# Kernel optimization log

Measured on AMD Instinct MI355X. Metric: run time of the kernel, lower is better.

Reference implementation:

```python
import jax, jax.numpy as jnp
import numpy as np

B, S, D, H, DN, DR, R = 2, 2048, 2048, 16, 32, 32, 128
HD = DN + DR  # head_dim = 64
EPS = 1e-5


def rms_norm(x, w):
    ms = jnp.mean(x * x, axis=-1, keepdims=True)
    return w * (x * jax.lax.rsqrt(ms + EPS))


def rotate_half(x):
    x1, x2 = x[..., : x.shape[-1] // 2], x[..., x.shape[-1] // 2:]
    return jnp.concatenate([-x2, x1], axis=-1)


def apply_rope(q, k, cos, sin):
    cos = cos[None, None]  # [1,1,S,DR]
    sin = sin[None, None]
    return q * cos + rotate_half(q) * sin, k * cos + rotate_half(k) * sin


def setup_inputs() -> dict:
    key = jax.random.key(0)
    ks = jax.random.split(key, 11)
    x = jax.random.normal(ks[0], (B, S, D), dtype=jnp.float32)
    # rotary tables
    pos = jnp.arange(S, dtype=jnp.float32)
    inv_freq = 1.0 / (10000.0 ** (jnp.arange(0, DR, 2, dtype=jnp.float32) / DR))
    ang = pos[:, None] * inv_freq[None, :]          # [S, DR/2]
    emb = jnp.concatenate([ang, ang], axis=-1)      # [S, DR]
    cos, sin = jnp.cos(emb), jnp.sin(emb)
    # causal additive mask
    mask = jnp.where(jnp.tril(jnp.ones((S, S), bool)), 0.0, -1e9).astype(jnp.float32)[None, None]
    s = 0.02
    return {
        "x": x, "cos": cos, "sin": sin, "mask": mask,
        "w_kv_down": jax.random.normal(ks[1], (D, R)) * s,
        "kv_norm_w": jnp.ones((R,), jnp.float32),
        "w_uk": jax.random.normal(ks[2], (R, H * DN)) * s,
        "w_ur": jax.random.normal(ks[3], (R, H * DR)) * s,
        "w_uv": jax.random.normal(ks[4], (R, H * HD)) * s,
        "w_q_down": jax.random.normal(ks[5], (D, R)) * s,
        "q_norm_w": jnp.ones((R,), jnp.float32),
        "w_uq": jax.random.normal(ks[6], (R, H * DN)) * s,
        "w_qr": jax.random.normal(ks[7], (R, H * DR)) * s,
        "w_o": jax.random.normal(ks[8], (H * HD, D)) * s,
    }


def reference(x, cos, sin, mask, w_kv_down, kv_norm_w, w_uk, w_ur, w_uv,
              w_q_down, q_norm_w, w_uq, w_qr, w_o):
    b, s, _ = x.shape

    def heads(t, hd):  # [b,s,H*hd] -> [b,H,s,hd]
        return t.reshape(b, s, H, hd).transpose(0, 2, 1, 3)

    c_kv = rms_norm(x @ w_kv_down, kv_norm_w)      # [b,s,R]
    k_nope = heads(c_kv @ w_uk, DN)
    k_rope = heads(c_kv @ w_ur, DR)
    v = heads(c_kv @ w_uv, HD)

    c_q = rms_norm(x @ w_q_down, q_norm_w)
    q_nope = heads(c_q @ w_uq, DN)
    q_rope = heads(c_q @ w_qr, DR)

    q_rope, k_rope = apply_rope(q_rope, k_rope, cos, sin)
    q = jnp.concatenate([q_nope, q_rope], axis=-1)  # [b,H,s,HD]
    k = jnp.concatenate([k_nope, k_rope], axis=-1)

    scores = jnp.einsum('bhqd,bhkd->bhqk', q, k) / jnp.sqrt(jnp.float32(HD))
    scores = scores + mask
    attn = jax.nn.softmax(scores, axis=-1)
    out = jnp.einsum('bhqk,bhkd->bhqd', attn, v)    # [b,H,s,HD]
    out = out.transpose(0, 2, 1, 3).reshape(b, s, H * HD)
    return out @ w_o
```

## Files before the change

### kernel.cpp

```cpp
#include <hip/hip_runtime.h>
#include <hip/hip_bf16.h>


using short8   = __attribute__((ext_vector_type(8))) short;
using bf16x8   = __attribute__((ext_vector_type(8))) __bf16;
using f32x4    = __attribute__((ext_vector_type(4))) float;
using f32x16   = __attribute__((ext_vector_type(16))) float;
using u32x4    = __attribute__((ext_vector_type(4))) unsigned;
using ushort4v = __attribute__((ext_vector_type(4))) unsigned short;

#define DEV __device__ __forceinline__

DEV ushort f2bf(float f) {
  union { float f; unsigned u; } v; v.f = f;
  unsigned r = (v.u + 0x7FFFu + ((v.u >> 16) & 1u)) >> 16;
  return (ushort)r;
}
DEV float bf2f(ushort u) {
  union { unsigned u; float f; } v; v.u = ((unsigned)u) << 16;
  return v.f;
}
DEV f32x4 mfma16(short8 a, short8 b, f32x4 c) {
  return __builtin_amdgcn_mfma_f32_16x16x32_bf16(
      __builtin_bit_cast(bf16x8, a), __builtin_bit_cast(bf16x8, b), c, 0, 0, 0);
}
DEV f32x16 mfma32(short8 a, short8 b, f32x16 c) {
  return __builtin_amdgcn_mfma_f32_32x32x16_bf16(
      __builtin_bit_cast(bf16x8, a), __builtin_bit_cast(bf16x8, b), c, 0, 0, 0);
}
DEV unsigned packbf(float a, float b) {
  return (unsigned)f2bf(a) | ((unsigned)f2bf(b) << 16);
}
DEV short8 mk8(unsigned a, unsigned b, unsigned c, unsigned d) {
  u32x4 t; t[0] = a; t[1] = b; t[2] = c; t[3] = d;
  return __builtin_bit_cast(short8, t);
}
DEV float vmax16(f32x16 v) {
  float a0 = fmaxf(v[0], v[1]),  a1 = fmaxf(v[2], v[3]);
  float a2 = fmaxf(v[4], v[5]),  a3 = fmaxf(v[6], v[7]);
  float a4 = fmaxf(v[8], v[9]),  a5 = fmaxf(v[10], v[11]);
  float a6 = fmaxf(v[12], v[13]), a7 = fmaxf(v[14], v[15]);
  float b0 = fmaxf(a0, a1), b1 = fmaxf(a2, a3), b2 = fmaxf(a4, a5), b3 = fmaxf(a6, a7);
  return fmaxf(fmaxf(b0, b1), fmaxf(b2, b3));
}
DEV float vsum16(f32x16 v) {
  float a0 = v[0] + v[1],  a1 = v[2] + v[3];
  float a2 = v[4] + v[5],  a3 = v[6] + v[7];
  float a4 = v[8] + v[9],  a5 = v[10] + v[11];
  float a6 = v[12] + v[13], a7 = v[14] + v[15];
  float b0 = a0 + a1, b1 = a2 + a3, b2 = a4 + a5, b3 = a6 + a7;
  return (b0 + b1) + (b2 + b3);
}

#define GLD16(gp, lp)                                                        \
  __builtin_amdgcn_global_load_lds(                                          \
      (const __attribute__((address_space(1))) void*)(gp),                   \
      (__attribute__((address_space(3))) void*)(lp), 16, 0, 0)

__global__ __launch_bounds__(256) void k_cast_bf16(const float* __restrict__ src,
                                                   ushort* __restrict__ dst, int n4) {
  int i = blockIdx.x * 256 + threadIdx.x;
  if (i < n4) {
    float4 v = reinterpret_cast<const float4*>(src)[i];
    ushort4v o;
    o[0] = f2bf(v.x); o[1] = f2bf(v.y); o[2] = f2bf(v.z); o[3] = f2bf(v.w);
    reinterpret_cast<ushort4v*>(dst)[i] = o;
  }
}

__global__ __launch_bounds__(256) void k_ttile(ushort* __restrict__ dst, int ldD,
                                               const float* __restrict__ src, int ldS) {
  __shared__ float t[64][65];
  const int k0 = blockIdx.x * 64, n0 = blockIdx.y * 64;
  const int c = threadIdx.x & 63, r0 = threadIdx.x >> 6;
#pragma unroll
  for (int i = 0; i < 16; ++i) {
    int r = r0 + i * 4;
    t[r][c] = src[(size_t)(k0 + r) * ldS + n0 + c];
  }
  __syncthreads();
#pragma unroll
  for (int i = 0; i < 16; ++i) {
    int n = r0 + i * 4;
    dst[(size_t)(n0 + n) * ldD + k0 + c] = f2bf(t[c][n]);
  }
}

template <int OUT_BF16>
__global__ __launch_bounds__(256) void k_gemm128(const ushort* __restrict__ A,
                                                 const ushort* __restrict__ Bt,
                                                 void* __restrict__ Cv, int N, int K) {
  __shared__ ushort As[128 * 64];
  __shared__ ushort Bs[128 * 64];
  const int tid = threadIdx.x;
  const int lane = tid & 63, w = tid >> 6;
  const int wr = w >> 1, wc = w & 1;
  const int r15 = lane & 15, g = lane >> 4;
  const size_t m0 = (size_t)blockIdx.y * 128;
  const size_t n0 = (size_t)blockIdx.x * 128;

  const ushort* pA = A + (m0 + w * 32 + (lane >> 3)) * K + (lane & 7) * 8;
  const ushort* pB = Bt + (n0 + w * 32 + (lane >> 3)) * K + (lane & 7) * 8;
  ushort* lA = &As[w * 2048];
  ushort* lB = &Bs[w * 2048];

  f32x4 acc[4][4] = {};
  for (int k0 = 0; k0 < K; k0 += 64) {
    __syncthreads();
#pragma unroll
    for (int c = 0; c < 4; ++c) GLD16(pA + (size_t)c * 8 * K + k0, lA + c * 512);
#pragma unroll
    for (int c = 0; c < 4; ++c) GLD16(pB + (size_t)c * 8 * K + k0, lB + c * 512);
    asm volatile("s_waitcnt vmcnt(0)" ::: "memory");
    __syncthreads();
#pragma unroll
    for (int kk = 0; kk < 2; ++kk) {
      short8 af[4], bf[4];
#pragma unroll
      for (int m = 0; m < 4; ++m)
        af[m] = *(const short8*)&As[(wr * 64 + m * 16 + r15) * 64 + kk * 32 + g * 8];
#pragma unroll
      for (int n = 0; n < 4; ++n)
        bf[n] = *(const short8*)&Bs[(wc * 64 + n * 16 + r15) * 64 + kk * 32 + g * 8];
#pragma unroll
      for (int m = 0; m < 4; ++m)
#pragma unroll
        for (int n = 0; n < 4; ++n)
          acc[m][n] = mfma16(af[m], bf[n], acc[m][n]);
    }
  }

#pragma unroll
  for (int m = 0; m < 4; ++m)
#pragma unroll
    for (int n = 0; n < 4; ++n)
#pragma unroll
      for (int j = 0; j < 4; ++j) {
        size_t row = m0 + wr * 64 + m * 16 + g * 4 + j;
        size_t col = n0 + wc * 64 + n * 16 + r15;
        float v = acc[m][n][j];
        if (OUT_BF16) ((ushort*)Cv)[row * N + col] = f2bf(v);
        else          ((float*)Cv)[row * N + col] = v;
      }
}

__global__ __launch_bounds__(256) void k_gemm128_sk(const ushort* __restrict__ A,
                                                    const ushort* __restrict__ Bt,
                                                    float* __restrict__ P, int N, int K) {
  __shared__ ushort As[128 * 64];
  __shared__ ushort Bs[128 * 64];
  const int tid = threadIdx.x;
  const int lane = tid & 63, w = tid >> 6;
  const int wr = w >> 1, wc = w & 1;
  const int r15 = lane & 15, g = lane >> 4;
  const size_t m0 = (size_t)blockIdx.y * 128;
  const size_t n0 = (size_t)blockIdx.x * 128;
  const int Ksub = K / gridDim.z;
  const int kbeg = blockIdx.z * Ksub, kend = kbeg + Ksub;
  const size_t plane = (size_t)blockIdx.z * gridDim.y * 128 * N;

  const ushort* pA = A + (m0 + w * 32 + (lane >> 3)) * K + (lane & 7) * 8;
  const ushort* pB = Bt + (n0 + w * 32 + (lane >> 3)) * K + (lane & 7) * 8;
  ushort* lA = &As[w * 2048];
  ushort* lB = &Bs[w * 2048];

  f32x4 acc[4][4] = {};
  for (int k0 = kbeg; k0 < kend; k0 += 64) {
    __syncthreads();
#pragma unroll
    for (int c = 0; c < 4; ++c) GLD16(pA + (size_t)c * 8 * K + k0, lA + c * 512);
#pragma unroll
    for (int c = 0; c < 4; ++c) GLD16(pB + (size_t)c * 8 * K + k0, lB + c * 512);
    asm volatile("s_waitcnt vmcnt(0)" ::: "memory");
    __syncthreads();
#pragma unroll
    for (int kk = 0; kk < 2; ++kk) {
      short8 af[4], bf[4];
#pragma unroll
      for (int m = 0; m < 4; ++m)
        af[m] = *(const short8*)&As[(wr * 64 + m * 16 + r15) * 64 + kk * 32 + g * 8];
#pragma unroll
      for (int n = 0; n < 4; ++n)
        bf[n] = *(const short8*)&Bs[(wc * 64 + n * 16 + r15) * 64 + kk * 32 + g * 8];
#pragma unroll
      for (int m = 0; m < 4; ++m)
#pragma unroll
        for (int n = 0; n < 4; ++n)
          acc[m][n] = mfma16(af[m], bf[n], acc[m][n]);
    }
  }

#pragma unroll
  for (int m = 0; m < 4; ++m)
#pragma unroll
    for (int n = 0; n < 4; ++n)
#pragma unroll
      for (int j = 0; j < 4; ++j) {
        size_t row = m0 + wr * 64 + m * 16 + g * 4 + j;
        size_t col = n0 + wc * 64 + n * 16 + r15;
        P[plane + row * N + col] = acc[m][n][j];
      }
}

__global__ __launch_bounds__(256) void k_red_rms(const float* __restrict__ P,
                                                 const float* __restrict__ wkv,
                                                 const float* __restrict__ wq,
                                                 ushort* __restrict__ ckv,
                                                 ushort* __restrict__ cq) {
  const int row = blockIdx.x, tid = threadIdx.x;
  const size_t MN = (size_t)4096 * 256;
  const size_t idx = (size_t)row * 256 + tid;
  float v = P[idx] + P[MN + idx] + P[2 * MN + idx] + P[3 * MN + idx];
  float sq = v * v;
#pragma unroll
  for (int d = 1; d < 64; d <<= 1) sq += __shfl_xor(sq, d, 64);
  __shared__ float red[4];
  if ((tid & 63) == 0) red[tid >> 6] = sq;
  __syncthreads();
  float ms = ((tid < 128) ? (red[0] + red[1]) : (red[2] + red[3])) * (1.0f / 128.0f);
  float r = rsqrtf(ms + 1e-5f);
  float w = (tid < 128) ? wkv[tid] : wq[tid - 128];
  ushort o = f2bf(v * r * w);
  if (tid < 128) ckv[(size_t)row * 128 + tid] = o;
  else           cq[(size_t)row * 128 + tid - 128] = o;
}

__global__ __launch_bounds__(256) void k_rope2(const ushort* __restrict__ kup,
                                               const ushort* __restrict__ qup,
                                               const float* __restrict__ cosT,
                                               const float* __restrict__ sinT,
                                               ushort* __restrict__ Kh,
                                               ushort* __restrict__ Qh) {
  const int row = blockIdx.x;
  const int b = row >> 11, s = row & 2047;
  const int t = threadIdx.x;
  const int hh = t >> 4, l16 = t & 15;
  const size_t dstb = ((size_t)(b * 16 + hh) * 2048 + s) * 64;
  ushort4v ko, qo;
  int d;
  if (l16 < 8) {
    d = l16 * 4;
    ushort4v kv = *(const ushort4v*)&kup[(size_t)row * 2048 + hh * 32 + d];
    ushort4v qv = *(const ushort4v*)&qup[(size_t)row * 1024 + hh * 32 + d];
    ko = kv;
#pragma unroll
    for (int i = 0; i < 4; ++i) qo[i] = f2bf(bf2f(qv[i]) * 0.125f);
  } else {
    const int r = (l16 - 8) * 4;
    d = 32 + r;
    float4 cv = *(const float4*)&cosT[s * 32 + r];
    float4 sv = *(const float4*)&sinT[s * 32 + r];
    const size_t bk = (size_t)row * 2048 + 512 + hh * 32;
    const size_t bq = (size_t)row * 1024 + 512 + hh * 32;
    ushort4v ka = *(const ushort4v*)&kup[bk + r];
    ushort4v qa = *(const ushort4v*)&qup[bq + r];
    const int rp = (r < 16) ? (r + 16) : (r - 16);
    const float sgn = (r < 16) ? -1.0f : 1.0f;
    ushort4v kb = *(const ushort4v*)&kup[bk + rp];
    ushort4v qb = *(const ushort4v*)&qup[bq + rp];
    float c[4] = {cv.x, cv.y, cv.z, cv.w};
    float sn[4] = {sv.x, sv.y, sv.z, sv.w};
#pragma unroll
    for (int i = 0; i < 4; ++i) {
      float kv_ = bf2f(ka[i]) * c[i] + sgn * bf2f(kb[i]) * sn[i];
      float qv_ = bf2f(qa[i]) * c[i] + sgn * bf2f(qb[i]) * sn[i];
      ko[i] = f2bf(kv_);
      qo[i] = f2bf(qv_ * 0.125f);
    }
  }
  *(ushort4v*)&Kh[dstb + d] = ko;
  *(ushort4v*)&Qh[dstb + d] = qo;
}

__global__ __launch_bounds__(256) void k_vtrans(const ushort* __restrict__ kup,
                                                ushort* __restrict__ Vt) {
  const int bh = blockIdx.y, b = bh >> 4, h = bh & 15;
  const int s0 = blockIdx.x * 64;
  __shared__ ushort t[64 * 64];
  const int tid = threadIdx.x;
  {
    const int sl = tid >> 2, ck = tid & 3;
    const ushort* src = &kup[(size_t)(b * 2048 + s0 + sl) * 2048 + 1024 + h * 64];
    short8 v0 = *(const short8*)(src + ck * 8);
    short8 v1 = *(const short8*)(src + (ck + 4) * 8);
    *(short8*)&t[sl * 64 + ((ck ^ (sl & 7)) * 8)] = v0;
    *(short8*)&t[sl * 64 + (((ck + 4) ^ (sl & 7)) * 8)] = v1;
  }
  __syncthreads();
  const int d = tid >> 2, sb = (tid & 3) * 16;
  ushort tmp[16];
#pragma unroll
  for (int i = 0; i < 16; ++i) {
    const int s = sb + i;
    tmp[i] = t[s * 64 + (((d >> 3) ^ (s & 7)) * 8) + (d & 7)];
  }
  ushort* dstp = &Vt[((size_t)bh * 64 + d) * 2048 + s0 + sb];
  *(short8*)(dstp)     = *(short8*)&tmp[0];
  *(short8*)(dstp + 8) = *(short8*)&tmp[8];
}

__global__ __launch_bounds__(256) void k_attn3(const ushort* __restrict__ Qh,
                                               const ushort* __restrict__ Kh,
                                               const ushort* __restrict__ Vt,
                                               ushort* __restrict__ AO) {
  const int bh = blockIdx.x;
  const int yy = blockIdx.y;
  const int gq = (yy & 1) ? (yy >> 1) : (31 - (yy >> 1));
  const int b = bh >> 4, h16 = bh & 15;
  const int tid = threadIdx.x, lane = tid & 63, w = tid >> 6;
  const int qc = w >> 1, s = w & 1;
  const int h = lane >> 5, q31 = lane & 31;
  const int q0 = gq * 64 + qc * 32;
  const int q = q0 + q31;
  const int nt = gq + 1;
  const int h1 = nt >> 1;
  const int jbeg = s ? (nt - h1) : 0;
  const int jend = s ? nt : (nt - h1);

  __shared__ float MR[2][64][36];

  const ushort* qbase = Qh + ((size_t)bh * 2048 + q) * 64 + 8 * h;
  short8 qf[4];
#pragma unroll
  for (int ds = 0; ds < 4; ++ds) qf[ds] = *(const short8*)(qbase + ds * 16);

  f32x16 oA = {}, oB = {};
  float m = -1e30f, l = 0.f;

  const ushort* Kb = Kh + (size_t)bh * 2048 * 64;
  const ushort* vA = Vt + ((size_t)bh * 64 + q31) * 2048;
  const ushort* vB = vA + (size_t)32 * 2048;

  for (int jt = jbeg; jt < jend; ++jt) {
    const int j0 = jt * 64;
    const ushort* kr0 = Kb + (size_t)(j0 + q31) * 64 + 8 * h;
    const ushort* kr1 = kr0 + 32 * 64;
    f32x16 sA = {}, sB = {};
#pragma unroll
    for (int ds = 0; ds < 4; ++ds) {
      sA = mfma32(*(const short8*)(kr0 + ds * 16), qf[ds], sA);
      sB = mfma32(*(const short8*)(kr1 + ds * 16), qf[ds], sB);
    }
    if (jt == nt - 1) {
      const int kb0 = j0 + 4 * h;
#pragma unroll
      for (int r = 0; r < 16; ++r) {
        const int key = kb0 + (r & 3) + 8 * (r >> 2);
        if (key > q) sA[r] = -1e30f;
        if (key + 32 > q) sB[r] = -1e30f;
      }
    }
    float mx = fmaxf(vmax16(sA), vmax16(sB));
    mx = fmaxf(mx, __shfl_xor(mx, 32, 64));
    if (!__all(mx <= m + 8.f)) {
      const float mn = fmaxf(m, mx);
      const float alpha = __expf(m - mn);
      m = mn;
      l *= alpha;
#pragma unroll
      for (int r = 0; r < 16; ++r) { oA[r] *= alpha; oB[r] *= alpha; }
    }
    f32x16 pA, pB;
#pragma unroll
    for (int r = 0; r < 16; ++r) pA[r] = __expf(sA[r] - m);
#pragma unroll
    for (int r = 0; r < 16; ++r) pB[r] = __expf(sB[r] - m);
    float rs = vsum16(pA) + vsum16(pB);
    rs += __shfl_xor(rs, 32, 64);
    l += rs;
    unsigned wa[8], wb[8];
#pragma unroll
    for (int j = 0; j < 8; ++j) wa[j] = packbf(pA[2 * j], pA[2 * j + 1]);
#pragma unroll
    for (int j = 0; j < 8; ++j) wb[j] = packbf(pB[2 * j], pB[2 * j + 1]);
    const bool hb = (h != 0);
    unsigned ra0 = (unsigned)__shfl_xor((int)(hb ? wa[0] : wa[2]), 32, 64);
    unsigned ra1 = (unsigned)__shfl_xor((int)(hb ? wa[1] : wa[3]), 32, 64);
    unsigned ra2 = (unsigned)__shfl_xor((int)(hb ? wa[4] : wa[6]), 32, 64);
    unsigned ra3 = (unsigned)__shfl_xor((int)(hb ? wa[5] : wa[7]), 32, 64);
    unsigned rb0 = (unsigned)__shfl_xor((int)(hb ? wb[0] : wb[2]), 32, 64);
    unsigned rb1 = (unsigned)__shfl_xor((int)(hb ? wb[1] : wb[3]), 32, 64);
    unsigned rb2 = (unsigned)__shfl_xor((int)(hb ? wb[4] : wb[6]), 32, 64);
    unsigned rb3 = (unsigned)__shfl_xor((int)(hb ? wb[5] : wb[7]), 32, 64);
    short8 pf00 = mk8(hb ? ra0 : wa[0], hb ? ra1 : wa[1], hb ? wa[2] : ra0, hb ? wa[3] : ra1);
    short8 pf01 = mk8(hb ? ra2 : wa[4], hb ? ra3 : wa[5], hb ? wa[6] : ra2, hb ? wa[7] : ra3);
    short8 pf10 = mk8(hb ? rb0 : wb[0], hb ? rb1 : wb[1], hb ? wb[2] : rb0, hb ? wb[3] : rb1);
    short8 pf11 = mk8(hb ? rb2 : wb[4], hb ? rb3 : wb[5], hb ? wb[6] : rb2, hb ? wb[7] : rb3);
    const ushort* vpA = vA + j0 + 8 * h;
    const ushort* vpB = vB + j0 + 8 * h;
    oA = mfma32(*(const short8*)(vpA +  0), pf00, oA);
    oB = mfma32(*(const short8*)(vpB +  0), pf00, oB);
    oA = mfma32(*(const short8*)(vpA + 16), pf01, oA);
    oB = mfma32(*(const short8*)(vpB + 16), pf01, oB);
    oA = mfma32(*(const short8*)(vpA + 32), pf10, oA);
    oB = mfma32(*(const short8*)(vpB + 32), pf10, oB);
    oA = mfma32(*(const short8*)(vpA + 48), pf11, oA);
    oB = mfma32(*(const short8*)(vpB + 48), pf11, oB);
  }

  if (s == 1) {
    MR[qc][lane][0] = m;
    MR[qc][lane][1] = l;
#pragma unroll
    for (int r = 0; r < 16; ++r) { MR[qc][lane][2 + r] = oA[r]; MR[qc][lane][18 + r] = oB[r]; }
  }
  __syncthreads();
  if (s == 0) {
    const float m1 = MR[qc][lane][0], l1 = MR[qc][lane][1];
    const float mm = fmaxf(m, m1);
    const float a0 = __expf(m - mm), a1 = __expf(m1 - mm);
    const float inv = 1.0f / (l * a0 + l1 * a1);
    ushort* dst = AO + ((size_t)b * 2048 + q) * 1024 + h16 * 64;
#pragma unroll
    for (int g4 = 0; g4 < 4; ++g4) {
      ushort4v pkA, pkB;
#pragma unroll
      for (int t2 = 0; t2 < 4; ++t2) {
        const int r = 4 * g4 + t2;
        pkA[t2] = f2bf((oA[r] * a0 + MR[qc][lane][2 + r] * a1) * inv);
        pkB[t2] = f2bf((oB[r] * a0 + MR[qc][lane][18 + r] * a1) * inv);
      }
      *(ushort4v*)(dst + 8 * g4 + 4 * h)      = pkA;
      *(ushort4v*)(dst + 8 * g4 + 4 * h + 32) = pkB;
    }
  }
}

extern "C" void kernel_launch(void* const* d_in, const int* in_sizes, int n_in,
                              void* d_out, int out_size, void* d_ws, size_t ws_size,
                              hipStream_t stream) {
  const float* x         = (const float*)d_in[0];
  const float* cosT      = (const float*)d_in[1];
  const float* sinT      = (const float*)d_in[2];
  const float* w_kv_down = (const float*)d_in[4];
  const float* kv_norm_w = (const float*)d_in[5];
  const float* w_uk      = (const float*)d_in[6];
  const float* w_ur      = (const float*)d_in[7];
  const float* w_uv      = (const float*)d_in[8];
  const float* w_q_down  = (const float*)d_in[9];
  const float* q_norm_w  = (const float*)d_in[10];
  const float* w_uq      = (const float*)d_in[11];
  const float* w_qr      = (const float*)d_in[12];
  const float* w_o       = (const float*)d_in[13];

  char* ws = (char*)d_ws;
  size_t off = 0;
  auto alloc = [&](size_t bytes) -> char* {
    char* p = ws + off;
    off += (bytes + 255) & ~(size_t)255;
    return p;
  };
  ushort* xb     = (ushort*)alloc(16777216);
  ushort* kup    = xb;
  ushort* qup    = (ushort*)alloc(8388608);
  ushort* Vt     = qup;
  ushort* wd_bT  = (ushort*)alloc(1048576);
  ushort* wu_kvT = (ushort*)alloc(524288);
  ushort* wu_qT  = (ushort*)alloc(262144);
  ushort* wo_bT  = (ushort*)alloc(4194304);
  ushort* ckv    = (ushort*)alloc(1048576);
  ushort* cq     = (ushort*)alloc(1048576);
  ushort* Kh     = (ushort*)alloc(8388608);
  ushort* Qh     = (ushort*)alloc(8388608);
  ushort* AO     = (ushort*)alloc(8388608);
  float*  pc1    = (float*)Kh;
  (void)ws_size; (void)in_sizes; (void)n_in; (void)out_size;

  k_cast_bf16<<<dim3(8192), dim3(256), 0, stream>>>(x, xb, 2097152);
  k_ttile<<<dim3(32, 2), dim3(256), 0, stream>>>(wd_bT, 2048, w_kv_down, 128);
  k_ttile<<<dim3(32, 2), dim3(256), 0, stream>>>(wd_bT + (size_t)128 * 2048, 2048, w_q_down, 128);
  k_ttile<<<dim3(2, 8), dim3(256), 0, stream>>>(wu_kvT, 128, w_uk, 512);
  k_ttile<<<dim3(2, 8), dim3(256), 0, stream>>>(wu_kvT + (size_t)512 * 128, 128, w_ur, 512);
  k_ttile<<<dim3(2, 16), dim3(256), 0, stream>>>(wu_kvT + (size_t)1024 * 128, 128, w_uv, 1024);
  k_ttile<<<dim3(2, 8), dim3(256), 0, stream>>>(wu_qT, 128, w_uq, 512);
  k_ttile<<<dim3(2, 8), dim3(256), 0, stream>>>(wu_qT + (size_t)512 * 128, 128, w_qr, 512);
  k_ttile<<<dim3(16, 32), dim3(256), 0, stream>>>(wo_bT, 1024, w_o, 2048);
  k_gemm128_sk<<<dim3(2, 32, 4), dim3(256), 0, stream>>>(xb, wd_bT, pc1, 256, 2048);
  k_red_rms<<<dim3(4096), dim3(256), 0, stream>>>(pc1, kv_norm_w, q_norm_w, ckv, cq);
  k_gemm128<1><<<dim3(16, 32), dim3(256), 0, stream>>>(ckv, wu_kvT, (void*)kup, 2048, 128);
  k_gemm128<1><<<dim3(8, 32), dim3(256), 0, stream>>>(cq, wu_qT, (void*)qup, 1024, 128);
  k_rope2<<<dim3(4096), dim3(256), 0, stream>>>(kup, qup, cosT, sinT, Kh, Qh);
  k_vtrans<<<dim3(32, 32), dim3(256), 0, stream>>>(kup, Vt);
  k_attn3<<<dim3(32, 32), dim3(256), 0, stream>>>(Qh, Kh, Vt, AO);
  k_gemm128<0><<<dim3(16, 32), dim3(256), 0, stream>>>(AO, wo_bT, d_out, 2048, 1024);
}
```

Measured before the change: 307.7 us.

## Stage K/V tiles in shared memory with double buffering; merge weight transposes

The attention kernel now lets each block handle 128 queries, four waves of 32 rows. All waves share K and V tiles that are copied into double-buffered, swizzled LDS with direct global-to-LDS loads, instead of each wave reading K/V straight from global memory. The split-KV partial merge through shared memory is removed, so each wave runs the whole causal range for its rows. The eight weight-transpose launches are folded into one kernel to cut launch overhead. The cost is that waves with fewer key tiles sit idle at barriers while others finish, and each block has less work split across it.

Result: faster. 258.8 us (-15.9%).

```diff
diff --git a/kernel.cpp b/kernel.cpp
--- a/kernel.cpp
+++ b/kernel.cpp
@@ -42,14 +42,6 @@
   float a6 = fmaxf(v[12], v[13]), a7 = fmaxf(v[14], v[15]);
   float b0 = fmaxf(a0, a1), b1 = fmaxf(a2, a3), b2 = fmaxf(a4, a5), b3 = fmaxf(a6, a7);
   return fmaxf(fmaxf(b0, b1), fmaxf(b2, b3));
-}
-DEV float vsum16(f32x16 v) {
-  float a0 = v[0] + v[1],  a1 = v[2] + v[3];
-  float a2 = v[4] + v[5],  a3 = v[6] + v[7];
-  float a4 = v[8] + v[9],  a5 = v[10] + v[11];
-  float a6 = v[12] + v[13], a7 = v[14] + v[15];
-  float b0 = a0 + a1, b1 = a2 + a3, b2 = a4 + a5, b3 = a6 + a7;
-  return (b0 + b1) + (b2 + b3);
 }
 
 #define GLD16(gp, lp)                                                        \
@@ -68,10 +60,25 @@
   }
 }
 
-__global__ __launch_bounds__(256) void k_ttile(ushort* __restrict__ dst, int ldD,
-                                               const float* __restrict__ src, int ldS) {
+__global__ __launch_bounds__(256) void k_ttile_all(
+    const float* __restrict__ s0, const float* __restrict__ s1,
+    const float* __restrict__ s2, const float* __restrict__ s3,
+    const float* __restrict__ s4, const float* __restrict__ s5,
+    const float* __restrict__ s6, const float* __restrict__ s7,
+    ushort* __restrict__ wd_bT, ushort* __restrict__ wu_kvT,
+    ushort* __restrict__ wu_qT, ushort* __restrict__ wo_bT) {
+  const int bid = blockIdx.x;
+  const float* src; ushort* dst; int ldS, ldD, nx, lb;
+  if (bid < 64)       { src = s0; dst = wd_bT;                       ldS = 128;  ldD = 2048; nx = 32; lb = bid; }
+  else if (bid < 128) { src = s1; dst = wd_bT + (size_t)128 * 2048;  ldS = 128;  ldD = 2048; nx = 32; lb = bid - 64; }
+  else if (bid < 144) { src = s2; dst = wu_kvT;                      ldS = 512;  ldD = 128;  nx = 2;  lb = bid - 128; }
+  else if (bid < 160) { src = s3; dst = wu_kvT + (size_t)512 * 128;  ldS = 512;  ldD = 128;  nx = 2;  lb = bid - 144; }
+  else if (bid < 192) { src = s4; dst = wu_kvT + (size_t)1024 * 128; ldS = 1024; ldD = 128;  nx = 2;  lb = bid - 160; }
+  else if (bid < 208) { src = s5; dst = wu_qT;                       ldS = 512;  ldD = 128;  nx = 2;  lb = bid - 192; }
+  else if (bid < 224) { src = s6; dst = wu_qT + (size_t)512 * 128;   ldS = 512;  ldD = 128;  nx = 2;  lb = bid - 208; }
+  else                { src = s7; dst = wo_bT;                       ldS = 2048; ldD = 1024; nx = 16; lb = bid - 224; }
+  const int k0 = (lb % nx) * 64, n0 = (lb / nx) * 64;
   __shared__ float t[64][65];
-  const int k0 = blockIdx.x * 64, n0 = blockIdx.y * 64;
   const int c = threadIdx.x & 63, r0 = threadIdx.x >> 6;
 #pragma unroll
   for (int i = 0; i < 16; ++i) {
@@ -299,25 +306,22 @@
   *(short8*)(dstp + 8) = *(short8*)&tmp[8];
 }
 
-__global__ __launch_bounds__(256) void k_attn3(const ushort* __restrict__ Qh,
+__global__ __launch_bounds__(256) void k_attn5(const ushort* __restrict__ Qh,
                                                const ushort* __restrict__ Kh,
                                                const ushort* __restrict__ Vt,
                                                ushort* __restrict__ AO) {
   const int bh = blockIdx.x;
-  const int yy = blockIdx.y;
-  const int gq = (yy & 1) ? (yy >> 1) : (31 - (yy >> 1));
+  const int cy = blockIdx.y;
+  const int c = (cy < 8) ? (15 - cy) : (cy - 8);
   const int b = bh >> 4, h16 = bh & 15;
   const int tid = threadIdx.x, lane = tid & 63, w = tid >> 6;
-  const int qc = w >> 1, s = w & 1;
   const int h = lane >> 5, q31 = lane & 31;
-  const int q0 = gq * 64 + qc * 32;
-  const int q = q0 + q31;
-  const int nt = gq + 1;
-  const int h1 = nt >> 1;
-  const int jbeg = s ? (nt - h1) : 0;
-  const int jend = s ? nt : (nt - h1);
-
-  __shared__ float MR[2][64][36];
+  const int qw0 = c * 128 + w * 32;
+  const int q = qw0 + q31;
+  const int mynt = (qw0 >> 6) + 1;
+  const int bnt = 2 * c + 2;
+
+  __shared__ ushort KV[2][8192];
 
   const ushort* qbase = Qh + ((size_t)bh * 2048 + q) * 64 + 8 * h;
   short8 qf[4];
@@ -327,102 +331,121 @@
   f32x16 oA = {}, oB = {};
   float m = -1e30f, l = 0.f;
 
-  const ushort* Kb = Kh + (size_t)bh * 2048 * 64;
-  const ushort* vA = Vt + ((size_t)bh * 64 + q31) * 2048;
-  const ushort* vB = vA + (size_t)32 * 2048;
-
-  for (int jt = jbeg; jt < jend; ++jt) {
-    const int j0 = jt * 64;
-    const ushort* kr0 = Kb + (size_t)(j0 + q31) * 64 + 8 * h;
-    const ushort* kr1 = kr0 + 32 * 64;
-    f32x16 sA = {}, sB = {};
-#pragma unroll
-    for (int ds = 0; ds < 4; ++ds) {
-      sA = mfma32(*(const short8*)(kr0 + ds * 16), qf[ds], sA);
-      sB = mfma32(*(const short8*)(kr1 + ds * 16), qf[ds], sB);
+  const ushort* Kg = Kh + (size_t)bh * 2048 * 64;
+  const ushort* Vg = Vt + (size_t)bh * 64 * 2048;
+
+  const int r0  = tid >> 3;
+  const int csh = ((tid & 7) ^ (r0 & 7)) << 3;
+  const int swz = (q31 & 7) << 4;
+  const int cxs = ((h << 4) ^ swz) >> 1;
+
+  auto stage = [&](int bi, int jtile) {
+    ushort* KD = &KV[bi][0];
+    ushort* VD = &KV[bi][4096];
+    const size_t kr = (size_t)(jtile * 64 + r0);
+    GLD16(Kg + kr * 64 + csh,                              KD + w * 512);
+    GLD16(Kg + (kr + 32) * 64 + csh,                       KD + 2048 + w * 512);
+    GLD16(Vg + (size_t)r0 * 2048 + jtile * 64 + csh,       VD + w * 512);
+    GLD16(Vg + (size_t)(32 + r0) * 2048 + jtile * 64 + csh, VD + 2048 + w * 512);
+  };
+
+  stage(0, 0);
+  for (int jt = 0; jt < bnt; ++jt) {
+    const int cur = jt & 1;
+    if (jt + 1 < bnt) {
+      stage(cur ^ 1, jt + 1);
+      asm volatile("s_waitcnt vmcnt(4)" ::: "memory");
+    } else {
+      asm volatile("s_waitcnt vmcnt(0)" ::: "memory");
     }
-    if (jt == nt - 1) {
-      const int kb0 = j0 + 4 * h;
-#pragma unroll
-      for (int r = 0; r < 16; ++r) {
-        const int key = kb0 + (r & 3) + 8 * (r >> 2);
-        if (key > q) sA[r] = -1e30f;
-        if (key + 32 > q) sB[r] = -1e30f;
-      }
+    __builtin_amdgcn_s_barrier();
+
+    if (jt < mynt) {
+      const int j0 = jt * 64;
+      const ushort* KL = &KV[cur][0];
+      const ushort* VL = &KV[cur][4096];
+      const ushort* kSa = KL + q31 * 64;
+      const ushort* kSb = KL + (32 + q31) * 64;
+      f32x16 sA = {}, sB = {};
+#pragma unroll
+      for (int ds = 0; ds < 4; ++ds) {
+        sA = mfma32(*(const short8*)(kSa + (cxs ^ (ds << 4))), qf[ds], sA);
+        sB = mfma32(*(const short8*)(kSb + (cxs ^ (ds << 4))), qf[ds], sB);
+      }
+      if (jt == mynt - 1) {
+        const int kb0 = j0 + 4 * h;
+#pragma unroll
+        for (int r = 0; r < 16; ++r) {
+          const int key = kb0 + (r & 3) + 8 * (r >> 2);
+          if (key > q) sA[r] = -1e30f;
+          if (key + 32 > q) sB[r] = -1e30f;
+        }
+      }
+      float mx = fmaxf(vmax16(sA), vmax16(sB));
+      mx = fmaxf(mx, __shfl_xor(mx, 32, 64));
+      if (!__all(mx <= m + 8.f)) {
+        const float mn = fmaxf(m, mx);
+        const float alpha = __expf(m - mn);
+        m = mn;
+        l *= alpha;
+#pragma unroll
+        for (int r = 0; r < 16; ++r) { oA[r] *= alpha; oB[r] *= alpha; }
+      }
+      float rs = 0.f;
+      unsigned wa[8], wb[8];
+#pragma unroll
+      for (int j2 = 0; j2 < 8; ++j2) {
+        float e0 = __expf(sA[2 * j2] - m), e1 = __expf(sA[2 * j2 + 1] - m);
+        rs += e0 + e1;
+        wa[j2] = packbf(e0, e1);
+      }
+#pragma unroll
+      for (int j2 = 0; j2 < 8; ++j2) {
+        float e0 = __expf(sB[2 * j2] - m), e1 = __expf(sB[2 * j2 + 1] - m);
+        rs += e0 + e1;
+        wb[j2] = packbf(e0, e1);
+      }
+      rs += __shfl_xor(rs, 32, 64);
+      l += rs;
+      const bool hb = (h != 0);
+      unsigned ra0 = (unsigned)__shfl_xor((int)(hb ? wa[0] : wa[2]), 32, 64);
+      unsigned ra1 = (unsigned)__shfl_xor((int)(hb ? wa[1] : wa[3]), 32, 64);
+      unsigned ra2 = (unsigned)__shfl_xor((int)(hb ? wa[4] : wa[6]), 32, 64);
+      unsigned ra3 = (unsigned)__shfl_xor((int)(hb ? wa[5] : wa[7]), 32, 64);
+      unsigned rb0 = (unsigned)__shfl_xor((int)(hb ? wb[0] : wb[2]), 32, 64);
+      unsigned rb1 = (unsigned)__shfl_xor((int)(hb ? wb[1] : wb[3]), 32, 64);
+      unsigned rb2 = (unsigned)__shfl_xor((int)(hb ? wb[4] : wb[6]), 32, 64);
+      unsigned rb3 = (unsigned)__shfl_xor((int)(hb ? wb[5] : wb[7]), 32, 64);
+      short8 pf00 = mk8(hb ? ra0 : wa[0], hb ? ra1 : wa[1], hb ? wa[2] : ra0, hb ? wa[3] : ra1);
+      short8 pf01 = mk8(hb ? ra2 : wa[4], hb ? ra3 : wa[5], hb ? wa[6] : ra2, hb ? wa[7] : ra3);
+      short8 pf10 = mk8(hb ? rb0 : wb[0], hb ? rb1 : wb[1], hb ? wb[2] : rb0, hb ? wb[3] : rb1);
+      short8 pf11 = mk8(hb ? rb2 : wb[4], hb ? rb3 : wb[5], hb ? wb[6] : rb2, hb ? wb[7] : rb3);
+      const ushort* vSa = VL + q31 * 64;
+      const ushort* vSb = VL + (32 + q31) * 64;
+      oA = mfma32(*(const short8*)(vSa + (cxs ^ 0)),  pf00, oA);
+      oA = mfma32(*(const short8*)(vSa + (cxs ^ 16)), pf01, oA);
+      oA = mfma32(*(const short8*)(vSa + (cxs ^ 32)), pf10, oA);
+      oA = mfma32(*(const short8*)(vSa + (cxs ^ 48)), pf11, oA);
+      oB = mfma32(*(const short8*)(vSb + (cxs ^ 0)),  pf00, oB);
+      oB = mfma32(*(const short8*)(vSb + (cxs ^ 16)), pf01, oB);
+      oB = mfma32(*(const short8*)(vSb + (cxs ^ 32)), pf10, oB);
+      oB = mfma32(*(const short8*)(vSb + (cxs ^ 48)), pf11, oB);
     }
-    float mx = fmaxf(vmax16(sA), vmax16(sB));
-    mx = fmaxf(mx, __shfl_xor(mx, 32, 64));
-    if (!__all(mx <= m + 8.f)) {
-      const float mn = fmaxf(m, mx);
-      const float alpha = __expf(m - mn);
-      m = mn;
-      l *= alpha;
-#pragma unroll
-      for (int r = 0; r < 16; ++r) { oA[r] *= alpha; oB[r] *= alpha; }
+    __builtin_amdgcn_s_barrier();
+  }
+
+  const float inv = 1.0f / l;
+  ushort* dst = AO + ((size_t)b * 2048 + q) * 1024 + h16 * 64;
+#pragma unroll
+  for (int g4 = 0; g4 < 4; ++g4) {
+    ushort4v pkA, pkB;
+#pragma unroll
+    for (int t2 = 0; t2 < 4; ++t2) {
+      pkA[t2] = f2bf(oA[4 * g4 + t2] * inv);
+      pkB[t2] = f2bf(oB[4 * g4 + t2] * inv);
     }
-    f32x16 pA, pB;
-#pragma unroll
-    for (int r = 0; r < 16; ++r) pA[r] = __expf(sA[r] - m);
-#pragma unroll
-    for (int r = 0; r < 16; ++r) pB[r] = __expf(sB[r] - m);
-    float rs = vsum16(pA) + vsum16(pB);
-    rs += __shfl_xor(rs, 32, 64);
-    l += rs;
-    unsigned wa[8], wb[8];
-#pragma unroll
-    for (int j = 0; j < 8; ++j) wa[j] = packbf(pA[2 * j], pA[2 * j + 1]);
-#pragma unroll
-    for (int j = 0; j < 8; ++j) wb[j] = packbf(pB[2 * j], pB[2 * j + 1]);
-    const bool hb = (h != 0);
-    unsigned ra0 = (unsigned)__shfl_xor((int)(hb ? wa[0] : wa[2]), 32, 64);
-    unsigned ra1 = (unsigned)__shfl_xor((int)(hb ? wa[1] : wa[3]), 32, 64);
-    unsigned ra2 = (unsigned)__shfl_xor((int)(hb ? wa[4] : wa[6]), 32, 64);
-    unsigned ra3 = (unsigned)__shfl_xor((int)(hb ? wa[5] : wa[7]), 32, 64);
-    unsigned rb0 = (unsigned)__shfl_xor((int)(hb ? wb[0] : wb[2]), 32, 64);
-    unsigned rb1 = (unsigned)__shfl_xor((int)(hb ? wb[1] : wb[3]), 32, 64);
-    unsigned rb2 = (unsigned)__shfl_xor((int)(hb ? wb[4] : wb[6]), 32, 64);
-    unsigned rb3 = (unsigned)__shfl_xor((int)(hb ? wb[5] : wb[7]), 32, 64);
-    short8 pf00 = mk8(hb ? ra0 : wa[0], hb ? ra1 : wa[1], hb ? wa[2] : ra0, hb ? wa[3] : ra1);
-    short8 pf01 = mk8(hb ? ra2 : wa[4], hb ? ra3 : wa[5], hb ? wa[6] : ra2, hb ? wa[7] : ra3);
-    short8 pf10 = mk8(hb ? rb0 : wb[0], hb ? rb1 : wb[1], hb ? wb[2] : rb0, hb ? wb[3] : rb1);
-    short8 pf11 = mk8(hb ? rb2 : wb[4], hb ? rb3 : wb[5], hb ? wb[6] : rb2, hb ? wb[7] : rb3);
-    const ushort* vpA = vA + j0 + 8 * h;
-    const ushort* vpB = vB + j0 + 8 * h;
-    oA = mfma32(*(const short8*)(vpA +  0), pf00, oA);
-    oB = mfma32(*(const short8*)(vpB +  0), pf00, oB);
-    oA = mfma32(*(const short8*)(vpA + 16), pf01, oA);
-    oB = mfma32(*(const short8*)(vpB + 16), pf01, oB);
-    oA = mfma32(*(const short8*)(vpA + 32), pf10, oA);
-    oB = mfma32(*(const short8*)(vpB + 32), pf10, oB);
-    oA = mfma32(*(const short8*)(vpA + 48), pf11, oA);
-    oB = mfma32(*(const short8*)(vpB + 48), pf11, oB);
-  }
-
-  if (s == 1) {
-    MR[qc][lane][0] = m;
-    MR[qc][lane][1] = l;
-#pragma unroll
-    for (int r = 0; r < 16; ++r) { MR[qc][lane][2 + r] = oA[r]; MR[qc][lane][18 + r] = oB[r]; }
-  }
-  __syncthreads();
-  if (s == 0) {
-    const float m1 = MR[qc][lane][0], l1 = MR[qc][lane][1];
-    const float mm = fmaxf(m, m1);
-    const float a0 = __expf(m - mm), a1 = __expf(m1 - mm);
-    const float inv = 1.0f / (l * a0 + l1 * a1);
-    ushort* dst = AO + ((size_t)b * 2048 + q) * 1024 + h16 * 64;
-#pragma unroll
-    for (int g4 = 0; g4 < 4; ++g4) {
-      ushort4v pkA, pkB;
-#pragma unroll
-      for (int t2 = 0; t2 < 4; ++t2) {
-        const int r = 4 * g4 + t2;
-        pkA[t2] = f2bf((oA[r] * a0 + MR[qc][lane][2 + r] * a1) * inv);
-        pkB[t2] = f2bf((oB[r] * a0 + MR[qc][lane][18 + r] * a1) * inv);
-      }
-      *(ushort4v*)(dst + 8 * g4 + 4 * h)      = pkA;
-      *(ushort4v*)(dst + 8 * g4 + 4 * h + 32) = pkB;
-    }
+    *(ushort4v*)(dst + 8 * g4 + 4 * h)      = pkA;
+    *(ushort4v*)(dst + 8 * g4 + 4 * h + 32) = pkB;
   }
 }
 
@@ -467,20 +490,15 @@
   (void)ws_size; (void)in_sizes; (void)n_in; (void)out_size;
 
   k_cast_bf16<<<dim3(8192), dim3(256), 0, stream>>>(x, xb, 2097152);
-  k_ttile<<<dim3(32, 2), dim3(256), 0, stream>>>(wd_bT, 2048, w_kv_down, 128);
-  k_ttile<<<dim3(32, 2), dim3(256), 0, stream>>>(wd_bT + (size_t)128 * 2048, 2048, w_q_down, 128);
-  k_ttile<<<dim3(2, 8), dim3(256), 0, stream>>>(wu_kvT, 128, w_uk, 512);
-  k_ttile<<<dim3(2, 8), dim3(256), 0, stream>>>(wu_kvT + (size_t)512 * 128, 128, w_ur, 512);
-  k_ttile<<<dim3(2, 16), dim3(256), 0, stream>>>(wu_kvT + (size_t)1024 * 128, 128, w_uv, 1024);
-  k_ttile<<<dim3(2, 8), dim3(256), 0, stream>>>(wu_qT, 128, w_uq, 512);
-  k_ttile<<<dim3(2, 8), dim3(256), 0, stream>>>(wu_qT + (size_t)512 * 128, 128, w_qr, 512);
-  k_ttile<<<dim3(16, 32), dim3(256), 0, stream>>>(wo_bT, 1024, w_o, 2048);
+  k_ttile_all<<<dim3(736), dim3(256), 0, stream>>>(
+      w_kv_down, w_q_down, w_uk, w_ur, w_uv, w_uq, w_qr, w_o,
+      wd_bT, wu_kvT, wu_qT, wo_bT);
   k_gemm128_sk<<<dim3(2, 32, 4), dim3(256), 0, stream>>>(xb, wd_bT, pc1, 256, 2048);
   k_red_rms<<<dim3(4096), dim3(256), 0, stream>>>(pc1, kv_norm_w, q_norm_w, ckv, cq);
   k_gemm128<1><<<dim3(16, 32), dim3(256), 0, stream>>>(ckv, wu_kvT, (void*)kup, 2048, 128);
   k_gemm128<1><<<dim3(8, 32), dim3(256), 0, stream>>>(cq, wu_qT, (void*)qup, 1024, 128);
   k_rope2<<<dim3(4096), dim3(256), 0, stream>>>(kup, qup, cosT, sinT, Kh, Qh);
   k_vtrans<<<dim3(32, 32), dim3(256), 0, stream>>>(kup, Vt);
-  k_attn3<<<dim3(32, 32), dim3(256), 0, stream>>>(Qh, Kh, Vt, AO);
+  k_attn5<<<dim3(32, 16), dim3(256), 0, stream>>>(Qh, Kh, Vt, AO);
   k_gemm128<0><<<dim3(16, 32), dim3(256), 0, stream>>>(AO, wo_bT, d_out, 2048, 1024);
 }
```
